# Kernel optimization log

Measured on AMD Instinct MI355X. Metric: run time of the kernel, lower is better.

## Reference

```python
import jax, jax.numpy as jnp
import numpy as np

B, S, H, A, E, ED, RH = 16, 2048, 1024, 32, 8, 256, 128  # batch, seq, hidden, act_dim, num_experts, expert_dim, router/aux hidden

def _mk(key, shape, scale=0.02):
    return (jax.random.normal(key, shape, dtype=jnp.float32) * scale)

def setup_inputs() -> dict:
    key = jax.random.key(0)
    ks = jax.random.split(key, 20)
    inp = {
        "state_rep": jax.random.normal(ks[0], (B, S, H), dtype=jnp.float32),
        "base_action": jax.random.normal(ks[1], (B, S, A), dtype=jnp.float32),
        "attention_mask": jnp.ones((B, S), dtype=jnp.float32),
        # shared expert
        "sw1": _mk(ks[2], (H, ED)), "sb1": jnp.zeros((ED,), jnp.float32),
        "sw2": _mk(ks[3], (ED, A)), "sb2": jnp.zeros((A,), jnp.float32),
        # stacked specialized experts
        "ew1": _mk(ks[4], (E, H, ED)), "eb1": jnp.zeros((E, ED), jnp.float32),
        "ew2": _mk(ks[5], (E, ED, A)), "eb2": jnp.zeros((E, A), jnp.float32),
        # router
        "rw1": _mk(ks[6], (H, RH)), "rb1": jnp.zeros((RH,), jnp.float32),
        "rw2": _mk(ks[7], (RH, E)), "rb2": jnp.zeros((E,), jnp.float32),
        # residual mlp
        "mw1": _mk(ks[8], (A, RH)), "mb1": jnp.zeros((RH,), jnp.float32),
        "mw2": _mk(ks[9], (RH, A)), "mb2": jnp.zeros((A,), jnp.float32),
        # value estimator
        "vw1": _mk(ks[10], (H, RH)), "vb1": jnp.zeros((RH,), jnp.float32),
        "vw2": _mk(ks[11], (RH, 1)), "vb2": jnp.zeros((1,), jnp.float32),
    }
    return inp

def reference(state_rep, base_action, attention_mask,
              sw1, sb1, sw2, sb2, ew1, eb1, ew2, eb2,
              rw1, rb1, rw2, rb2, mw1, mb1, mw2, mb2,
              vw1, vb1, vw2, vb2):
    gelu = lambda x: jax.nn.gelu(x, approximate=False)  # torch nn.GELU default (erf)
    # value estimator -> sigmoid RTG  [B,S,1]
    return_rtg = jax.nn.sigmoid(jax.nn.relu(state_rep @ vw1 + vb1) @ vw2 + vb2)
    # shared expert [B,S,A]
    shared_output = gelu(state_rep @ sw1 + sb1) @ sw2 + sb2
    # candidate actions [B,S,E,A]
    scaling = jnp.linspace(0.8, 1.2, E, dtype=jnp.float32).reshape(1, 1, E, 1)
    candidate_actions = base_action[:, :, None, :] * scaling
    # router softmax [B,S,E]
    router_logits = gelu(state_rep @ rw1 + rb1) @ rw2 + rb2
    selection_probs = jax.nn.softmax(router_logits, axis=-1)
    # all experts on all tokens (matches the training-mode torch loop)
    h1 = gelu(jnp.einsum('bsh,ehd->bsed', state_rep, ew1) + eb1[None, None, :, :])
    expert_outputs = jnp.einsum('bsed,eda->bsea', h1, ew2) + eb2[None, None, :, :]
    # training branch: soft combine
    weighted_expert = jnp.sum(selection_probs[..., None] * expert_outputs, axis=2)
    moe_output = shared_output + weighted_expert
    residual = gelu(moe_output @ mw1 + mb1) @ mw2 + mb2
    final_action = weighted_expert + residual
    final_action = final_action * attention_mask[..., None]
    return (final_action, candidate_actions, selection_probs, return_rtg)
```

## Files before the change

kernel.cpp:

```cpp
#include <hip/hip_runtime.h>
#include <stdint.h>

#define T_TOT 32768
#define H_DIM 1024
#define A_DIM 32
#define E_NUM 8
#define ED_DIM 256
#define RH_DIM 128
#define NBIG 2560
#define K2 2304

typedef float f32x4 __attribute__((ext_vector_type(4)));
typedef short bf16x8 __attribute__((ext_vector_type(8)));
typedef unsigned short u16;
typedef u16 u16x8 __attribute__((ext_vector_type(8)));

typedef uint32_t __attribute__((address_space(1))) as1_u32;
typedef uint32_t __attribute__((address_space(3))) as3_u32;

__device__ __forceinline__ u16 f2bf(float f) {
    union { float f; uint32_t u; } v; v.f = f;
    return (u16)((v.u + 0x7FFFu + ((v.u >> 16) & 1u)) >> 16);
}
__device__ __forceinline__ float bf2f(u16 h) {
    union { uint32_t u; float f; } v; v.u = ((uint32_t)h) << 16;
    return v.f;
}
__device__ __forceinline__ float gelu_fast(float x) {
    const float x2 = x * x;
    const float s = x * fmaf(0.07135481627f, x2, 1.5957691216f);
    const float e = __expf(-s);
    return x * __builtin_amdgcn_rcpf(1.0f + e);
}
__device__ __forceinline__ void gload_lds16(const void* g, void* lds) {
    __builtin_amdgcn_global_load_lds((const as1_u32*)(uintptr_t)g,
                                     (as3_u32*)(uintptr_t)lds, 16, 0, 0);
}


__global__ void k_packwt(const float* __restrict__ ew1, const float* __restrict__ sw1,
                         const float* __restrict__ rw1, const float* __restrict__ vw1,
                         u16* __restrict__ wbf) {
    __shared__ float t[64][65];
    const int nt = blockIdx.x >> 4, kt = blockIdx.x & 15;
    const int n0 = nt * 64, k0 = kt * 64;
    const int tx = threadIdx.x & 63, ty = threadIdx.x >> 6;
#pragma unroll 4
    for (int it = 0; it < 16; ++it) {
        const int k = k0 + ty + it * 4;
        const int n = n0 + tx;
        float v;
        if (n0 < 2048)      v = ew1[(size_t)((n0 >> 8) * H_DIM + k) * ED_DIM + (n & 255)];
        else if (n0 < 2304) v = sw1[(size_t)k * ED_DIM + (n - 2048)];
        else if (n0 < 2432) v = rw1[(size_t)k * RH_DIM + (n - 2304)];
        else                v = vw1[(size_t)k * RH_DIM + (n - 2432)];
        t[ty + it * 4][tx] = v;
    }
    __syncthreads();
#pragma unroll 4
    for (int it = 0; it < 16; ++it) {
        const int nl = ty + it * 4;
        wbf[(size_t)(n0 + nl) * H_DIM + k0 + tx] = f2bf(t[tx][nl]);
    }
}


#define SB_W2T (A_DIM * K2)
#define SB_W1B (SB_W2T + 4096)
#define SB_W2B (SB_W1B + 4352)
#define SB_BIA (SB_W2B + NBIG)
#define SB_CND (SB_BIA + T_TOT * E_NUM * A_DIM)

__global__ void k_setup(const float* __restrict__ eb1, const float* __restrict__ sb1,
                        const float* __restrict__ rb1, const float* __restrict__ vb1,
                        const float* __restrict__ ew2, const float* __restrict__ sw2,
                        const float* __restrict__ mw1, const float* __restrict__ mw2,
                        const float* __restrict__ base, const float* __restrict__ state,
                        float* __restrict__ biascat,
                        u16* __restrict__ w2t, u16* __restrict__ w1b, u16* __restrict__ w2b,
                        float* __restrict__ cand_out, u16* __restrict__ xb, int nconv4) {
    int i = blockIdx.x * blockDim.x + threadIdx.x;
    if (i < SB_W2T) {
        int a = i / K2, d = i - a * K2;
        float v = (d < 2048) ? ew2[(size_t)d * A_DIM + a] : sw2[(size_t)(d - 2048) * A_DIM + a];
        w2t[i] = f2bf(v);
    } else if (i < SB_W1B) {
        int t = i - SB_W2T;
        w1b[t] = f2bf(mw1[t]);
    } else if (i < SB_W2B) {
        int t = i - SB_W1B;
        int c = t / 136, j = t - c * 136;
        w2b[t] = (j < RH_DIM) ? f2bf(mw2[(size_t)j * A_DIM + c]) : (u16)0;
    } else if (i < SB_BIA) {
        int n = i - SB_W2B;
        float b;
        if (n < 2048)      b = eb1[(n >> 8) * ED_DIM + (n & 255)];
        else if (n < 2304) b = sb1[n - 2048];
        else if (n < 2432) b = rb1[n - 2304];
        else               b = vb1[n - 2432];
        biascat[n] = b;
    } else if (i < SB_CND) {
        int t = i - SB_BIA;
        int a = t & 31, e = (t >> 5) & 7, tt = t >> 8;
        cand_out[t] = base[(size_t)tt * A_DIM + a] * (0.8f + 0.4f * (float)e / 7.0f);
    } else if (i < SB_CND + nconv4) {
        int t = i - SB_CND;
        float4 v = ((const float4*)state)[t];
        ushort4 o;
        o.x = f2bf(v.x); o.y = f2bf(v.y); o.z = f2bf(v.z); o.w = f2bf(v.w);
        ((ushort4*)xb)[t] = o;
    }
}

__global__ void k_convert_x(const float* __restrict__ x, u16* __restrict__ xb, int n4) {
    int i = blockIdx.x * blockDim.x + threadIdx.x;
    if (i >= n4) return;
    float4 v = ((const float4*)x)[i];
    ushort4 o;
    o.x = f2bf(v.x); o.y = f2bf(v.y); o.z = f2bf(v.z); o.w = f2bf(v.w);
    ((ushort4*)xb)[i] = o;
}


#define SLOT 8192

__launch_bounds__(512, 2)
__global__ void k_gemm1(const u16* __restrict__ xb, const u16* __restrict__ wbf,
                        const float* __restrict__ biascat, u16* __restrict__ h1,
                        const float* __restrict__ rw2, const float* __restrict__ rb2,
                        const float* __restrict__ vw2, const float* __restrict__ vb2,
                        float* __restrict__ probs_out, float* __restrict__ rtg_out) {
    __shared__ u16 smem[8 * SLOT];
    __shared__ float rw2s[RH_DIM * E_NUM];
    __shared__ float vws[RH_DIM];
    __shared__ float rb2s[E_NUM];
    const int tid = threadIdx.x;
    const int wid = tid >> 6;
    const int lane = tid & 63;
    const int lin = blockIdx.x;
    const int swz = (lin & 7) * ((int)gridDim.x >> 3) + (lin >> 3);
    const int bx = swz % 10;
    const int by = swz / 10;
    const int m0 = by * 256, n0 = bx * 256;
    const int wr = wid >> 2;
    const int wc = wid & 3;
    const int srow = tid >> 3;
    const int cs = 8 * ((tid & 7) ^ (srow & 7));
    const int l15 = lane & 15;
    const int rsw = (lane & 7) * 8;
    const int lh8 = (lane >> 4) * 8;
    const int c0 = lh8 ^ rsw;
    const int c1 = (32 + lh8) ^ rsw;
    const int aRd = (wr * 16 + l15) * 64;
    const int bRd = ((wc & 1) * 64 + l15) * 64;
    const int bSlotHi = wc >> 1;

    f32x4 acc[8][4];
#pragma unroll
    for (int j = 0; j < 8; ++j)
#pragma unroll
        for (int n = 0; n < 4; ++n) acc[j][n] = (f32x4){0.f, 0.f, 0.f, 0.f};

    auto stageA = [&](int h, int kt, int s) {
        const u16* src = xb + (size_t)(m0 + h * 128 + srow) * H_DIM + kt * 64 + cs;
        u16* dst = smem + s * SLOT + wid * 512;
        gload_lds16(src, dst);
        gload_lds16(src + (size_t)64 * H_DIM, dst + 4096);
    };
    auto stageB = [&](int h, int kt, int s) {
        const u16* src = wbf + (size_t)(n0 + h * 128 + srow) * H_DIM + kt * 64 + cs;
        u16* dst = smem + s * SLOT + wid * 512;
        gload_lds16(src, dst);
        gload_lds16(src + (size_t)64 * H_DIM, dst + 4096);
    };

    bf16x8 bfr[4][2];

#define G1_READA(q, P, A0, A1)                                                    \
    {                                                                             \
        const u16* ab0 = smem + ((P) * 4 + ((q) >> 1)) * SLOT + aRd + (((2*(q)) & 3) * 2048);     \
        const u16* ab1 = smem + ((P) * 4 + ((q) >> 1)) * SLOT + aRd + (((2*(q)+1) & 3) * 2048);   \
        A0[0] = *(const bf16x8*)&ab0[c0]; A0[1] = *(const bf16x8*)&ab0[c1];       \
        A1[0] = *(const bf16x8*)&ab1[c0]; A1[1] = *(const bf16x8*)&ab1[c1];       \
    }

#define G1_MFMA(q, A0, A1)                                                        \
    _Pragma("unroll")                                                             \
    for (int ni = 0; ni < 4; ++ni) {                                              \
        acc[2*(q)][ni]   = __builtin_amdgcn_mfma_f32_16x16x32_bf16(A0[0], bfr[ni][0], acc[2*(q)][ni], 0, 0, 0);   \
        acc[2*(q)][ni]   = __builtin_amdgcn_mfma_f32_16x16x32_bf16(A0[1], bfr[ni][1], acc[2*(q)][ni], 0, 0, 0);   \
        acc[2*(q)+1][ni] = __builtin_amdgcn_mfma_f32_16x16x32_bf16(A1[0], bfr[ni][0], acc[2*(q)+1][ni], 0, 0, 0); \
        acc[2*(q)+1][ni] = __builtin_amdgcn_mfma_f32_16x16x32_bf16(A1[1], bfr[ni][1], acc[2*(q)+1][ni], 0, 0, 0); \
    }

    stageB(0, 0, 2); stageB(1, 0, 3);
    stageA(0, 0, 0); stageA(1, 0, 1);
    stageB(0, 1, 6); stageB(1, 1, 7);
    asm volatile("s_waitcnt vmcnt(6)" ::: "memory");
    __builtin_amdgcn_s_barrier();

#pragma unroll 2
    for (int kt = 0; kt < 16; ++kt) {
        const int p = kt & 1;
        const int ktA = (kt + 1) & 15;
        const int ktB = (kt + 2) & 15;
        const int pA = ktA & 1;
        bf16x8 a0[2], a1[2];
        G1_READA(0, p, a0, a1)
#pragma unroll
        for (int ni = 0; ni < 4; ++ni) {
            const u16* bb = smem + (p * 4 + 2 + bSlotHi) * SLOT + bRd + ni * 1024;
            bfr[ni][0] = *(const bf16x8*)&bb[c0];
            bfr[ni][1] = *(const bf16x8*)&bb[c1];
        }
        stageA(0, ktA, pA * 4);
        __builtin_amdgcn_s_barrier();
        asm volatile("s_waitcnt lgkmcnt(0)" ::: "memory");
        __builtin_amdgcn_sched_barrier(0);
        __builtin_amdgcn_s_setprio(1);
        G1_MFMA(0, a0, a1)
        __builtin_amdgcn_s_setprio(0);
        G1_READA(1, p, a0, a1)
        stageA(1, ktA, pA * 4 + 1);
        asm volatile("s_waitcnt vmcnt(8)" ::: "memory");
        __builtin_amdgcn_s_barrier();
        asm volatile("s_waitcnt lgkmcnt(0)" ::: "memory");
        __builtin_amdgcn_sched_barrier(0);
        __builtin_amdgcn_s_setprio(1);
        G1_MFMA(1, a0, a1)
        __builtin_amdgcn_s_setprio(0);
        G1_READA(2, p, a0, a1)
        stageB(0, ktB, p * 4 + 2);
        __builtin_amdgcn_s_barrier();
        asm volatile("s_waitcnt lgkmcnt(0)" ::: "memory");
        __builtin_amdgcn_sched_barrier(0);
        __builtin_amdgcn_s_setprio(1);
        G1_MFMA(2, a0, a1)
        __builtin_amdgcn_s_setprio(0);
        G1_READA(3, p, a0, a1)
        stageB(1, ktB, p * 4 + 3);
        asm volatile("s_waitcnt vmcnt(6)" ::: "memory");
        __builtin_amdgcn_s_barrier();
        asm volatile("s_waitcnt lgkmcnt(0)" ::: "memory");
        __builtin_amdgcn_sched_barrier(0);
        __builtin_amdgcn_s_setprio(1);
        G1_MFMA(3, a0, a1)
        __builtin_amdgcn_s_setprio(0);
    }
#undef G1_READA
#undef G1_MFMA

    const int crow = (lane >> 4) * 4;
    if (bx != 9) {
#pragma unroll
        for (int j = 0; j < 8; ++j) {
#pragma unroll
            for (int ni = 0; ni < 4; ++ni) {
                const int col = n0 + wc * 64 + ni * 16 + l15;
                const float bias = biascat[col];
#pragma unroll
                for (int r = 0; r < 4; ++r) {
                    const int row = m0 + wr * 16 + j * 32 + crow + r;
                    h1[(size_t)row * NBIG + col] = f2bf(gelu_fast(acc[j][ni][r] + bias));
                }
            }
        }
    } else {
        __syncthreads();
        for (int i = tid; i < RH_DIM * E_NUM; i += 512) rw2s[i] = rw2[i];
        if (tid < RH_DIM) vws[tid] = vw2[tid];
        if (tid < E_NUM) rb2s[tid] = rb2[tid];
        char* sb = (char*)smem;
#pragma unroll
        for (int j = 0; j < 8; ++j) {
#pragma unroll
            for (int ni = 0; ni < 4; ++ni) {
                const int col = wc * 64 + ni * 16 + l15;
                const float bias = biascat[2304 + col];
#pragma unroll
                for (int r = 0; r < 4; ++r) {
                    const int row = wr * 16 + j * 32 + crow + r;
                    float v = acc[j][ni][r] + bias;
                    v = (col < 128) ? gelu_fast(v) : fmaxf(v, 0.f);
                    *(u16*)(sb + row * 512 + ((col * 2) ^ ((row & 31) << 4))) = f2bf(v);
                }
            }
        }
        __syncthreads();
        if (tid < 256) {
            const int row = tid;
            float lg[E_NUM];
#pragma unroll
            for (int e = 0; e < E_NUM; ++e) lg[e] = rb2s[e];
            const int rx = (row & 31) << 4;
#pragma unroll 4
            for (int s = 0; s < 16; ++s) {
                u16x8 v8 = *(const u16x8*)(sb + row * 512 + ((s << 4) ^ rx));
#pragma unroll
                for (int q = 0; q < 8; ++q) {
                    const float xv = bf2f(v8[q]);
                    const float* wr8 = &rw2s[(s * 8 + q) * E_NUM];
#pragma unroll
                    for (int e = 0; e < E_NUM; ++e) lg[e] = fmaf(xv, wr8[e], lg[e]);
                }
            }
            float mx = lg[0];
#pragma unroll
            for (int e = 1; e < E_NUM; ++e) mx = fmaxf(mx, lg[e]);
            float sm = 0.f;
            float ex[E_NUM];
#pragma unroll
            for (int e = 0; e < E_NUM; ++e) { ex[e] = __expf(lg[e] - mx); sm += ex[e]; }
            const float rs = 1.0f / sm;
#pragma unroll
            for (int e = 0; e < E_NUM; ++e) probs_out[(size_t)(m0 + row) * E_NUM + e] = ex[e] * rs;
        } else {
            const int row = tid - 256;
            const int rx = (row & 31) << 4;
            float pv = 0.f;
#pragma unroll 4
            for (int s = 16; s < 32; ++s) {
                u16x8 v8 = *(const u16x8*)(sb + row * 512 + ((s << 4) ^ rx));
#pragma unroll
                for (int q = 0; q < 8; ++q) pv = fmaf(bf2f(v8[q]), vws[(s - 16) * 8 + q], pv);
            }
            rtg_out[m0 + row] = 1.f / (1.f + __expf(-(pv + vb2[0])));
        }
    }
}


__launch_bounds__(256, 3)
__global__ void k_gemm2(const u16* __restrict__ h1, const u16* __restrict__ w2t,
                        const float* __restrict__ probs,
                        const float* __restrict__ eb2, const float* __restrict__ sb2,
                        const u16* __restrict__ w1b, const u16* __restrict__ w2b,
                        const float* __restrict__ mb1, const float* __restrict__ mb2,
                        const float* __restrict__ mask, float* __restrict__ out_final) {
    __shared__ u16 uni[12288];
    __shared__ float plds[64 * E_NUM];
    __shared__ u16 w1s[32 * 128];
    __shared__ u16 w2s[32 * 136];
    const int tid = threadIdx.x;
    const int wid = tid >> 6;
    const int lane = tid & 63;
    const int m0 = blockIdx.x * 64;
    const int csrc = 8 * ((tid & 7) ^ ((tid >> 3) & 7));
    const int rxor = (lane & 7) * 8;
    const int lhi8 = (lane >> 4) * 8;
    const int crow = (lane >> 4) * 4;
    const int ccol = lane & 15;

    for (int i = tid; i < 64 * E_NUM; i += 256) plds[i] = probs[(size_t)m0 * E_NUM + i];
    for (int i = tid; i < 4096; i += 256) w1s[i] = w1b[i];
    for (int i = tid; i < 544; i += 256) *(u16x8*)&w2s[i * 8] = *(const u16x8*)&w2b[i * 8];

    f32x4 accE[2], accT[2], accS[2];
#pragma unroll
    for (int n = 0; n < 2; ++n) {
        accE[n] = (f32x4){0.f, 0.f, 0.f, 0.f};
        accT[n] = (f32x4){0.f, 0.f, 0.f, 0.f};
        accS[n] = (f32x4){0.f, 0.f, 0.f, 0.f};
    }

    auto stage = [&](int buf, int kt) {
        const int k0 = kt * 64;
#pragma unroll
        for (int j = 0; j < 2; ++j)
            gload_lds16(h1 + (size_t)(m0 + j * 32 + (tid >> 3)) * NBIG + k0 + csrc,
                        &uni[buf * 4096 + j * 2048 + wid * 512]);
        gload_lds16(w2t + (size_t)(tid >> 3) * K2 + k0 + csrc, &uni[8192 + buf * 2048 + wid * 512]);
    };

    stage(0, 0);
    __syncthreads();
    int cur = 0;
    for (int kt = 0; kt < 36; ++kt) {
        if (kt < 35) stage(cur ^ 1, kt + 1);
        const bool isExp = (kt < 32);
#pragma unroll
        for (int kk = 0; kk < 64; kk += 32) {
            bf16x8 av = *(const bf16x8*)&uni[cur * 4096 + (wid * 16 + (lane & 15)) * 64 + ((kk + lhi8) ^ rxor)];
            bf16x8 bv0 = *(const bf16x8*)&uni[8192 + cur * 2048 + ((lane & 15)) * 64 + ((kk + lhi8) ^ rxor)];
            bf16x8 bv1 = *(const bf16x8*)&uni[8192 + cur * 2048 + (16 + (lane & 15)) * 64 + ((kk + lhi8) ^ rxor)];
            if (isExp) {
                accE[0] = __builtin_amdgcn_mfma_f32_16x16x32_bf16(av, bv0, accE[0], 0, 0, 0);
                accE[1] = __builtin_amdgcn_mfma_f32_16x16x32_bf16(av, bv1, accE[1], 0, 0, 0);
            } else {
                accS[0] = __builtin_amdgcn_mfma_f32_16x16x32_bf16(av, bv0, accS[0], 0, 0, 0);
                accS[1] = __builtin_amdgcn_mfma_f32_16x16x32_bf16(av, bv1, accS[1], 0, 0, 0);
            }
        }
        if (isExp && (kt & 3) == 3) {
            const int e = kt >> 2;
#pragma unroll
            for (int r = 0; r < 4; ++r) {
                const float p = plds[(wid * 16 + crow + r) * E_NUM + e];
#pragma unroll
                for (int n = 0; n < 2; ++n) {
                    accT[n][r] += p * accE[n][r];
                    accE[n][r] = 0.f;
                }
            }
        }
        __syncthreads();
        cur ^= 1;
    }

    u16* Am = uni;
    u16* rhm = uni + 2560;
    float wgt[2][4];
#pragma unroll
    for (int n = 0; n < 2; ++n) {
        const int aIdx = n * 16 + ccol;
#pragma unroll
        for (int r = 0; r < 4; ++r) {
            const int row = wid * 16 + crow + r;
            float wb = 0.f;
#pragma unroll
            for (int e = 0; e < E_NUM; ++e) wb += plds[row * E_NUM + e] * eb2[e * A_DIM + aIdx];
            const float w = accT[n][r] + wb;
            wgt[n][r] = w;
            Am[row * 40 + aIdx] = f2bf(w + accS[n][r] + sb2[aIdx]);
        }
    }
    __syncthreads();
    {
        const int row = tid >> 2, seg = tid & 3;
        float mrow[32];
#pragma unroll
        for (int a = 0; a < 32; ++a) mrow[a] = bf2f(Am[row * 40 + a]);
#pragma unroll 4
        for (int jj = 0; jj < 32; ++jj) {
            const int j = seg * 32 + jj;
            float s = mb1[j];
#pragma unroll
            for (int a = 0; a < 32; ++a) s = fmaf(mrow[a], bf2f(w1s[a * 128 + j]), s);
            rhm[row * 136 + j] = f2bf(gelu_fast(s));
        }
    }
    __syncthreads();
#pragma unroll
    for (int n = 0; n < 2; ++n) {
        const int aIdx = n * 16 + ccol;
        const float b2 = mb2[aIdx];
#pragma unroll
        for (int r = 0; r < 4; ++r) {
            const int row = wid * 16 + crow + r;
            float s = b2;
#pragma unroll
            for (int jc = 0; jc < 16; ++jc) {
                u16x8 rv = *(const u16x8*)&rhm[row * 136 + jc * 8];
                u16x8 wv = *(const u16x8*)&w2s[aIdx * 136 + jc * 8];
#pragma unroll
                for (int q = 0; q < 8; ++q) s = fmaf(bf2f(rv[q]), bf2f(wv[q]), s);
            }
            const int t = m0 + row;
            out_final[(size_t)t * A_DIM + aIdx] = (wgt[n][r] + s) * mask[t];
        }
    }
}


extern "C" void kernel_launch(void* const* d_in, const int* in_sizes, int n_in,
                              void* d_out, int out_size, void* d_ws, size_t ws_size,
                              hipStream_t stream) {
    const float* state = (const float*)d_in[0];
    const float* base  = (const float*)d_in[1];
    const float* mask  = (const float*)d_in[2];
    const float* sw1 = (const float*)d_in[3];
    const float* sb1 = (const float*)d_in[4];
    const float* sw2 = (const float*)d_in[5];
    const float* sb2 = (const float*)d_in[6];
    const float* ew1 = (const float*)d_in[7];
    const float* eb1 = (const float*)d_in[8];
    const float* ew2 = (const float*)d_in[9];
    const float* eb2 = (const float*)d_in[10];
    const float* rw1 = (const float*)d_in[11];
    const float* rb1 = (const float*)d_in[12];
    const float* rw2 = (const float*)d_in[13];
    const float* rb2 = (const float*)d_in[14];
    const float* mw1 = (const float*)d_in[15];
    const float* mb1 = (const float*)d_in[16];
    const float* mw2 = (const float*)d_in[17];
    const float* mb2 = (const float*)d_in[18];
    const float* vw1 = (const float*)d_in[19];
    const float* vb1 = (const float*)d_in[20];
    const float* vw2 = (const float*)d_in[21];
    const float* vb2 = (const float*)d_in[22];

    float* out_final = (float*)d_out;
    float* out_cand  = out_final + 1048576;
    float* out_probs = out_final + 9437184;
    float* out_rtg   = out_final + 9699328;

    auto al = [](size_t b) { return (b + 255) & ~(size_t)255; };
    auto need = [&](size_t T) {
        return al((size_t)NBIG * H_DIM * 2) + al((size_t)A_DIM * K2 * 2) + al((size_t)NBIG * 4)
             + al((size_t)4096 * 2) + al((size_t)4352 * 2)
             + al(T * H_DIM * 2) + al(T * NBIG * 2);
    };
    size_t Tc = 8192;
    if (need(32768) <= ws_size)      Tc = 32768;
    else if (need(16384) <= ws_size) Tc = 16384;
    const int nchunk = (int)(T_TOT / Tc);

    char* ws = (char*)d_ws;
    size_t off = 0;
    auto take = [&](size_t b) { char* p = ws + off; off += (b + 255) & ~(size_t)255; return p; };
    u16*   wbf   = (u16*)take((size_t)NBIG * H_DIM * 2);
    u16*   w2t   = (u16*)take((size_t)A_DIM * K2 * 2);
    float* bias  = (float*)take((size_t)NBIG * 4);
    u16*   w1b   = (u16*)take((size_t)4096 * 2);
    u16*   w2b   = (u16*)take((size_t)4352 * 2);
    u16*   xb    = (u16*)take(Tc * H_DIM * 2);
    u16*   h1    = (u16*)take(Tc * NBIG * 2);
    (void)in_sizes; (void)n_in; (void)out_size;

    const int nconv4 = (Tc == 32768) ? (T_TOT * H_DIM / 4) : 0;
    const int ntot = SB_CND + nconv4;
    k_packwt<<<640, 256, 0, stream>>>(ew1, sw1, rw1, vw1, wbf);
    k_setup<<<(ntot + 255) / 256, 256, 0, stream>>>(
        eb1, sb1, rb1, vb1, ew2, sw2, mw1, mw2,
        base, state, bias, w2t, w1b, w2b, out_cand, xb, nconv4);

    for (int c = 0; c < nchunk; ++c) {
        const size_t tb = (size_t)c * Tc;
        if (nconv4 == 0)
            k_convert_x<<<(int)(Tc * H_DIM / 4 / 256), 256, 0, stream>>>(state + tb * H_DIM, xb, (int)(Tc * H_DIM / 4));
        k_gemm1<<<10 * (int)(Tc / 256), 512, 0, stream>>>(xb, wbf, bias, h1,
                                                          rw2, rb2, vw2, vb2,
                                                          out_probs + tb * E_NUM, out_rtg + tb);
        k_gemm2<<<(int)(Tc / 64), 256, 0, stream>>>(h1, w2t, out_probs + tb * E_NUM, eb2, sb2,
                                                    w1b, w2b, mb1, mb2, mask + tb, out_final + tb * A_DIM);
    }
}
```

Before: 290.9 us.

## Fuse second expert GEMM into gemm1 epilogue, emit per-expert partial outputs

The GEMM1 epilogue now keeps each 256x256 gelu'd hidden tile in shared memory and multiplies it by the matching slice of the second-layer weights with MFMA. It writes fp32 per-expert partial outputs (9x32 per token) instead of the full bf16 h1 activation matrix. The second kernel becomes a light combine that applies router probabilities, biases and the residual MLP. This removes writing and re-reading a 32768x2560 bf16 intermediate, at the cost of extra epilogue work and an added barrier in gemm1, plus uncoalesced w2t loads from global memory.

```diff
diff --git a/kernel.cpp b/kernel.cpp
--- a/kernel.cpp
+++ b/kernel.cpp
@@ -126,7 +126,8 @@
 
 __launch_bounds__(512, 2)
 __global__ void k_gemm1(const u16* __restrict__ xb, const u16* __restrict__ wbf,
-                        const float* __restrict__ biascat, u16* __restrict__ h1,
+                        const float* __restrict__ biascat, const u16* __restrict__ w2t,
+                        float* __restrict__ Pb,
                         const float* __restrict__ rw2, const float* __restrict__ rb2,
                         const float* __restrict__ vw2, const float* __restrict__ vb2,
                         float* __restrict__ probs_out, float* __restrict__ rtg_out) {
@@ -251,22 +252,56 @@
 #undef G1_MFMA
 
     const int crow = (lane >> 4) * 4;
+    __syncthreads();
     if (bx != 9) {
 #pragma unroll
         for (int j = 0; j < 8; ++j) {
 #pragma unroll
             for (int ni = 0; ni < 4; ++ni) {
-                const int col = n0 + wc * 64 + ni * 16 + l15;
-                const float bias = biascat[col];
+                const int col = wc * 64 + ni * 16 + l15;
+                const float bias = biascat[n0 + col];
 #pragma unroll
                 for (int r = 0; r < 4; ++r) {
-                    const int row = m0 + wr * 16 + j * 32 + crow + r;
-                    h1[(size_t)row * NBIG + col] = f2bf(gelu_fast(acc[j][ni][r] + bias));
+                    const int row = wr * 16 + j * 32 + crow + r;
+                    const float v = gelu_fast(acc[j][ni][r] + bias);
+                    smem[row * 256 + ((((col >> 3) ^ (row & 15)) << 3) | (col & 7))] = f2bf(v);
                 }
             }
         }
+        __syncthreads();
+        f32x4 accP[2][2];
+#pragma unroll
+        for (int m = 0; m < 2; ++m)
+#pragma unroll
+            for (int n = 0; n < 2; ++n) accP[m][n] = (f32x4){0.f, 0.f, 0.f, 0.f};
+        const int lh16 = lane >> 4;
+#pragma unroll
+        for (int g = 0; g < 8; ++g) {
+            bf16x8 bv[2], av[2];
+#pragma unroll
+            for (int ni = 0; ni < 2; ++ni)
+                bv[ni] = *(const bf16x8*)(w2t + (size_t)(ni * 16 + l15) * K2 + n0 + g * 32 + lh16 * 8);
+#pragma unroll
+            for (int m = 0; m < 2; ++m) {
+                const int row = wid * 32 + m * 16 + l15;
+                av[m] = *(const bf16x8*)&smem[row * 256 + (((g * 4 + lh16) ^ l15) << 3)];
+            }
+#pragma unroll
+            for (int m = 0; m < 2; ++m)
+#pragma unroll
+                for (int ni = 0; ni < 2; ++ni)
+                    accP[m][ni] = __builtin_amdgcn_mfma_f32_16x16x32_bf16(av[m], bv[ni], accP[m][ni], 0, 0, 0);
+        }
+#pragma unroll
+        for (int m = 0; m < 2; ++m)
+#pragma unroll
+            for (int ni = 0; ni < 2; ++ni)
+#pragma unroll
+                for (int r = 0; r < 4; ++r) {
+                    const int row = m0 + wid * 32 + m * 16 + crow + r;
+                    Pb[((size_t)row * 9 + bx) * 32 + ni * 16 + l15] = accP[m][ni][r];
+                }
     } else {
-        __syncthreads();
         for (int i = tid; i < RH_DIM * E_NUM; i += 512) rw2s[i] = rw2[i];
         if (tid < RH_DIM) vws[tid] = vw2[tid];
         if (tid < E_NUM) rb2s[tid] = rb2[tid];
@@ -331,84 +366,28 @@
 
 
 __launch_bounds__(256, 3)
-__global__ void k_gemm2(const u16* __restrict__ h1, const u16* __restrict__ w2t,
-                        const float* __restrict__ probs,
-                        const float* __restrict__ eb2, const float* __restrict__ sb2,
-                        const u16* __restrict__ w1b, const u16* __restrict__ w2b,
-                        const float* __restrict__ mb1, const float* __restrict__ mb2,
-                        const float* __restrict__ mask, float* __restrict__ out_final) {
-    __shared__ u16 uni[12288];
+__global__ void k_combine(const float* __restrict__ Pb, const float* __restrict__ probs,
+                          const float* __restrict__ eb2, const float* __restrict__ sb2,
+                          const u16* __restrict__ w1b, const u16* __restrict__ w2b,
+                          const float* __restrict__ mb1, const float* __restrict__ mb2,
+                          const float* __restrict__ mask, float* __restrict__ out_final) {
     __shared__ float plds[64 * E_NUM];
+    __shared__ u16 Am[64 * 40];
+    __shared__ u16 rhm[64 * 136];
     __shared__ u16 w1s[32 * 128];
     __shared__ u16 w2s[32 * 136];
     const int tid = threadIdx.x;
     const int wid = tid >> 6;
     const int lane = tid & 63;
     const int m0 = blockIdx.x * 64;
-    const int csrc = 8 * ((tid & 7) ^ ((tid >> 3) & 7));
-    const int rxor = (lane & 7) * 8;
-    const int lhi8 = (lane >> 4) * 8;
     const int crow = (lane >> 4) * 4;
     const int ccol = lane & 15;
 
     for (int i = tid; i < 64 * E_NUM; i += 256) plds[i] = probs[(size_t)m0 * E_NUM + i];
     for (int i = tid; i < 4096; i += 256) w1s[i] = w1b[i];
     for (int i = tid; i < 544; i += 256) *(u16x8*)&w2s[i * 8] = *(const u16x8*)&w2b[i * 8];
-
-    f32x4 accE[2], accT[2], accS[2];
-#pragma unroll
-    for (int n = 0; n < 2; ++n) {
-        accE[n] = (f32x4){0.f, 0.f, 0.f, 0.f};
-        accT[n] = (f32x4){0.f, 0.f, 0.f, 0.f};
-        accS[n] = (f32x4){0.f, 0.f, 0.f, 0.f};
-    }
-
-    auto stage = [&](int buf, int kt) {
-        const int k0 = kt * 64;
-#pragma unroll
-        for (int j = 0; j < 2; ++j)
-            gload_lds16(h1 + (size_t)(m0 + j * 32 + (tid >> 3)) * NBIG + k0 + csrc,
-                        &uni[buf * 4096 + j * 2048 + wid * 512]);
-        gload_lds16(w2t + (size_t)(tid >> 3) * K2 + k0 + csrc, &uni[8192 + buf * 2048 + wid * 512]);
-    };
-
-    stage(0, 0);
     __syncthreads();
-    int cur = 0;
-    for (int kt = 0; kt < 36; ++kt) {
-        if (kt < 35) stage(cur ^ 1, kt + 1);
-        const bool isExp = (kt < 32);
-#pragma unroll
-        for (int kk = 0; kk < 64; kk += 32) {
-            bf16x8 av = *(const bf16x8*)&uni[cur * 4096 + (wid * 16 + (lane & 15)) * 64 + ((kk + lhi8) ^ rxor)];
-            bf16x8 bv0 = *(const bf16x8*)&uni[8192 + cur * 2048 + ((lane & 15)) * 64 + ((kk + lhi8) ^ rxor)];
-            bf16x8 bv1 = *(const bf16x8*)&uni[8192 + cur * 2048 + (16 + (lane & 15)) * 64 + ((kk + lhi8) ^ rxor)];
-            if (isExp) {
-                accE[0] = __builtin_amdgcn_mfma_f32_16x16x32_bf16(av, bv0, accE[0], 0, 0, 0);
-                accE[1] = __builtin_amdgcn_mfma_f32_16x16x32_bf16(av, bv1, accE[1], 0, 0, 0);
-            } else {
-                accS[0] = __builtin_amdgcn_mfma_f32_16x16x32_bf16(av, bv0, accS[0], 0, 0, 0);
-                accS[1] = __builtin_amdgcn_mfma_f32_16x16x32_bf16(av, bv1, accS[1], 0, 0, 0);
-            }
-        }
-        if (isExp && (kt & 3) == 3) {
-            const int e = kt >> 2;
-#pragma unroll
-            for (int r = 0; r < 4; ++r) {
-                const float p = plds[(wid * 16 + crow + r) * E_NUM + e];
-#pragma unroll
-                for (int n = 0; n < 2; ++n) {
-                    accT[n][r] += p * accE[n][r];
-                    accE[n][r] = 0.f;
-                }
-            }
-        }
-        __syncthreads();
-        cur ^= 1;
-    }
-
-    u16* Am = uni;
-    u16* rhm = uni + 2560;
+
     float wgt[2][4];
 #pragma unroll
     for (int n = 0; n < 2; ++n) {
@@ -416,12 +395,13 @@
 #pragma unroll
         for (int r = 0; r < 4; ++r) {
             const int row = wid * 16 + crow + r;
-            float wb = 0.f;
-#pragma unroll
-            for (int e = 0; e < E_NUM; ++e) wb += plds[row * E_NUM + e] * eb2[e * A_DIM + aIdx];
-            const float w = accT[n][r] + wb;
+            const float* pt = Pb + (size_t)(m0 + row) * 288;
+            float w = 0.f;
+#pragma unroll
+            for (int e = 0; e < E_NUM; ++e)
+                w = fmaf(plds[row * E_NUM + e], pt[e * 32 + aIdx] + eb2[e * A_DIM + aIdx], w);
             wgt[n][r] = w;
-            Am[row * 40 + aIdx] = f2bf(w + accS[n][r] + sb2[aIdx]);
+            Am[row * 40 + aIdx] = f2bf(w + pt[256 + aIdx] + sb2[aIdx]);
         }
     }
     __syncthreads();
@@ -498,7 +478,7 @@
     auto need = [&](size_t T) {
         return al((size_t)NBIG * H_DIM * 2) + al((size_t)A_DIM * K2 * 2) + al((size_t)NBIG * 4)
              + al((size_t)4096 * 2) + al((size_t)4352 * 2)
-             + al(T * H_DIM * 2) + al(T * NBIG * 2);
+             + al(T * H_DIM * 2) + al(T * 9 * A_DIM * 4);
     };
     size_t Tc = 8192;
     if (need(32768) <= ws_size)      Tc = 32768;
@@ -514,7 +494,7 @@
     u16*   w1b   = (u16*)take((size_t)4096 * 2);
     u16*   w2b   = (u16*)take((size_t)4352 * 2);
     u16*   xb    = (u16*)take(Tc * H_DIM * 2);
-    u16*   h1    = (u16*)take(Tc * NBIG * 2);
+    float* Pb    = (float*)take(Tc * 9 * A_DIM * 4);
     (void)in_sizes; (void)n_in; (void)out_size;
 
     const int nconv4 = (Tc == 32768) ? (T_TOT * H_DIM / 4) : 0;
@@ -528,10 +508,10 @@
         const size_t tb = (size_t)c * Tc;
         if (nconv4 == 0)
             k_convert_x<<<(int)(Tc * H_DIM / 4 / 256), 256, 0, stream>>>(state + tb * H_DIM, xb, (int)(Tc * H_DIM / 4));
-        k_gemm1<<<10 * (int)(Tc / 256), 512, 0, stream>>>(xb, wbf, bias, h1,
+        k_gemm1<<<10 * (int)(Tc / 256), 512, 0, stream>>>(xb, wbf, bias, w2t, Pb,
                                                           rw2, rb2, vw2, vb2,
                                                           out_probs + tb * E_NUM, out_rtg + tb);
-        k_gemm2<<<(int)(Tc / 64), 256, 0, stream>>>(h1, w2t, out_probs + tb * E_NUM, eb2, sb2,
-                                                    w1b, w2b, mb1, mb2, mask + tb, out_final + tb * A_DIM);
-    }
-}
+        k_combine<<<(int)(Tc / 64), 256, 0, stream>>>(Pb, out_probs + tb * E_NUM, eb2, sb2,
+                                                      w1b, w2b, mb1, mb2, mask + tb, out_final + tb * A_DIM);
+    }
+}
```

Result: faster. 274.8 us (-5.5%).
